# Optimization experiments

Measured on AMD Instinct MI355X. Metric: run time of the kernel, lower is better.

Reference implementation:

```python
import jax, jax.numpy as jnp
import numpy as np

K, D = 512, 64


def setup_inputs() -> dict:
    key = jax.random.key(0)
    k1, k2 = jax.random.split(key)
    z_e_x = jax.random.normal(k1, (32, 4096, D), dtype=jnp.float32)
    # nn.Embedding weight initialized uniform(-1/K, 1/K)
    codebook = jax.random.uniform(k2, (K, D), dtype=jnp.float32,
                                  minval=-1.0 / K, maxval=1.0 / K)
    return {"z_e_x": z_e_x, "codebook": codebook}


def reference(z_e_x, codebook):
    # vq(): pairwise squared L2 distances to codebook, then argmin.
    d = z_e_x.shape[-1]
    flat = z_e_x.reshape(-1, d)                                   # [N, D]
    # ||z||^2 - 2 z.e + ||e||^2  (addmm form from original vq)
    dists = (jnp.sum(flat * flat, axis=1, keepdims=True)
             - 2.0 * flat @ codebook.T
             + jnp.sum(codebook * codebook, axis=1))              # [N, K]
    indices = jnp.argmin(dists, axis=1)                            # [N]
    # latents: indices reshaped to input shape minus feature dim
    return indices.reshape(z_e_x.shape[:-1])
```

## Files before the change

kernel.cpp:

```cpp
#include <hip/hip_runtime.h>
#include <math.h>

#define K_CODES 512
#define D_DIM   64
#define BM      512
#define THREADS 512
#define LSTR    72
#define EPS_GAP 4e-5f

#define WS_CNT_OFF  2048
#define WS_EH_OFF   4096
#define WS_EL_OFF   77824
#define WS_LIST_OFF 151552

typedef __attribute__((ext_vector_type(8))) short short8v;
typedef __attribute__((ext_vector_type(4))) float f32x4;

__device__ __forceinline__ float np_sumsq64(const float* zarr) {
    float L[16];
#pragma unroll
    for (int j = 0; j < 16; ++j)
        L[j] = __fadd_rn(
            __fadd_rn(__fmul_rn(zarr[j],      zarr[j]),
                      __fmul_rn(zarr[j + 16], zarr[j + 16])),
            __fadd_rn(__fmul_rn(zarr[j + 32], zarr[j + 32]),
                      __fmul_rn(zarr[j + 48], zarr[j + 48])));
    float m[8];
#pragma unroll
    for (int j = 0; j < 8; ++j) m[j] = __fadd_rn(L[j], L[j + 8]);
    float n4[4];
#pragma unroll
    for (int j = 0; j < 4; ++j) n4[j] = __fadd_rn(m[j], m[j + 4]);
    return __fadd_rn(__fadd_rn(n4[0], n4[2]), __fadd_rn(n4[1], n4[3]));
}

__device__ __forceinline__ unsigned short f32_bf16_rne(float x) {
    unsigned int u = __float_as_uint(x);
    unsigned int r = (u + 0x7FFFu + ((u >> 16) & 1u)) >> 16;
    return (unsigned short)r;
}
__device__ __forceinline__ float bf16_f32(unsigned short h) {
    return __uint_as_float(((unsigned int)h) << 16);
}
__device__ __forceinline__ void split2(float x, unsigned short& h, unsigned short& l) {
    h = f32_bf16_rne(x);
    l = f32_bf16_rne(x - bf16_f32(h));
}

__global__ __launch_bounds__(256)
void vq_prep_kernel(const float* __restrict__ cb, float* __restrict__ ws,
                    int do_split) {
    int g = blockIdx.x * blockDim.x + threadIdx.x;
    if (g == 0) *reinterpret_cast<int*>((char*)ws + WS_CNT_OFF) = 0;
    int k = g >> 2, q = g & 3;
    if (k >= K_CODES) return;
    const float* row = cb + (size_t)k * D_DIM;
    if (q == 0) {
        float e[D_DIM];
        const float4* p = reinterpret_cast<const float4*>(row);
#pragma unroll
        for (int i = 0; i < 16; ++i) {
            float4 v = p[i];
            e[4*i+0]=v.x; e[4*i+1]=v.y; e[4*i+2]=v.z; e[4*i+3]=v.w;
        }
        ws[k] = np_sumsq64(e);
    }
    if (do_split) {
        unsigned short* eh = reinterpret_cast<unsigned short*>((char*)ws + WS_EH_OFF)
                             + (size_t)k * LSTR;
        unsigned short* el = reinterpret_cast<unsigned short*>((char*)ws + WS_EL_OFF)
                             + (size_t)k * LSTR;
#pragma unroll
        for (int i = 16 * q; i < 16 * q + 16; ++i) {
            unsigned short h, l;
            split2(row[i], h, l);
            eh[i] = h; el[i] = l;
        }
        if (q == 3)
#pragma unroll
            for (int i = D_DIM; i < LSTR; ++i) { eh[i] = 0; el[i] = 0; }
    }
}

__global__ __launch_bounds__(512)
void vq_pass1_mono(const float* __restrict__ z,
                   const unsigned short* __restrict__ eh_g,
                   const unsigned short* __restrict__ el_g,
                   const float* __restrict__ norms, int* __restrict__ out,
                   int* __restrict__ cnt, int* __restrict__ list, int cap, int n) {
    __shared__ __align__(16) unsigned short ehS[K_CODES * LSTR];
    __shared__ __align__(16) unsigned short elS[K_CODES * LSTR];
    __shared__ __align__(16) float nrmS[K_CODES];

    const int tid  = threadIdx.x;
    const int l    = tid & 63;
    const int w    = tid >> 6;
    const int j    = l >> 4;
    const int c16  = l & 15;
    const int base = blockIdx.x * BM;

    {
        const char* esrc = (const char*)eh_g;
        const char* lsrc = (const char*)el_g;
#pragma unroll
        for (int r = 0; r < 9; ++r) {
            size_t off = ((size_t)tid + (size_t)r * THREADS) * 16;
            __builtin_amdgcn_global_load_lds(
                (const __attribute__((address_space(1))) void*)(esrc + off),
                (__attribute__((address_space(3))) void*)((char*)ehS + off), 16, 0, 0);
            __builtin_amdgcn_global_load_lds(
                (const __attribute__((address_space(1))) void*)(lsrc + off),
                (__attribute__((address_space(3))) void*)((char*)elS + off), 16, 0, 0);
        }
        if (tid < K_CODES / 4)
            reinterpret_cast<float4*>(nrmS)[tid] =
                reinterpret_cast<const float4*>(norms)[tid];
    }

    short8v bzh[4][2], bzl[4][2];
#pragma unroll
    for (int p = 0; p < 4; ++p) {
        int row = base + (4 * w + p) * 16 + c16;
        if (row >= n) row = n - 1;
        const float* zp = z + (size_t)row * D_DIM + j * 8;
#pragma unroll
        for (int h = 0; h < 2; ++h) {
            float4 v0 = *reinterpret_cast<const float4*>(zp + h * 32);
            float4 v1 = *reinterpret_cast<const float4*>(zp + h * 32 + 4);
            unsigned short hh[8], ll[8];
            split2(v0.x, hh[0], ll[0]); split2(v0.y, hh[1], ll[1]);
            split2(v0.z, hh[2], ll[2]); split2(v0.w, hh[3], ll[3]);
            split2(v1.x, hh[4], ll[4]); split2(v1.y, hh[5], ll[5]);
            split2(v1.z, hh[6], ll[6]); split2(v1.w, hh[7], ll[7]);
            short8v th, tl;
#pragma unroll
            for (int i = 0; i < 8; ++i) { th[i] = (short)hh[i]; tl[i] = (short)ll[i]; }
            bzh[p][h] = th; bzl[p][h] = tl;
        }
    }

    __syncthreads();

    float m1[4] = {INFINITY, INFINITY, INFINITY, INFINITY};
    float m2[4] = {INFINITY, INFINITY, INFINITY, INFINITY};
    int   i1[4] = {0, 0, 0, 0};

#pragma unroll 4
    for (int ct = 0; ct < 32; ++ct) {
        int ar = (ct * 16 + c16) * LSTR + j * 8;
        short8v aeh0 = *reinterpret_cast<const short8v*>(&ehS[ar]);
        short8v aeh1 = *reinterpret_cast<const short8v*>(&ehS[ar + 32]);
        short8v ael0 = *reinterpret_cast<const short8v*>(&elS[ar]);
        short8v ael1 = *reinterpret_cast<const short8v*>(&elS[ar + 32]);
        float4 nr = *reinterpret_cast<const float4*>(&nrmS[ct * 16 + j * 4]);
        float nra[4] = {nr.x, nr.y, nr.z, nr.w};
        int kg0 = ct * 16 + j * 4;
#pragma unroll
        for (int p = 0; p < 4; ++p) {
            f32x4 acc = {0.f, 0.f, 0.f, 0.f};
            acc = __builtin_amdgcn_mfma_f32_16x16x32_bf16(aeh0, bzh[p][0], acc, 0, 0, 0);
            acc = __builtin_amdgcn_mfma_f32_16x16x32_bf16(aeh1, bzh[p][1], acc, 0, 0, 0);
            acc = __builtin_amdgcn_mfma_f32_16x16x32_bf16(aeh0, bzl[p][0], acc, 0, 0, 0);
            acc = __builtin_amdgcn_mfma_f32_16x16x32_bf16(aeh1, bzl[p][1], acc, 0, 0, 0);
            acc = __builtin_amdgcn_mfma_f32_16x16x32_bf16(ael0, bzh[p][0], acc, 0, 0, 0);
            acc = __builtin_amdgcn_mfma_f32_16x16x32_bf16(ael1, bzh[p][1], acc, 0, 0, 0);
#pragma unroll
            for (int r = 0; r < 4; ++r) {
                float s = fmaf(-2.0f, acc[r], nra[r]);
                int kg = kg0 + r;
                bool lt1 = s < m1[p];
                float nm2 = lt1 ? m1[p] : fminf(s, m2[p]);
                i1[p] = lt1 ? kg : i1[p];
                m1[p] = lt1 ? s : m1[p];
                m2[p] = nm2;
            }
        }
    }

#pragma unroll
    for (int p = 0; p < 4; ++p) {
        float a1 = m1[p], a2 = m2[p]; int ai = i1[p];
#pragma unroll
        for (int off = 16; off <= 32; off <<= 1) {
            float o1 = __shfl_xor(a1, off, 64);
            float o2 = __shfl_xor(a2, off, 64);
            int   oi = __shfl_xor(ai, off, 64);
            float hi = fmaxf(a1, o1);
            bool take = o1 < a1;
            ai = take ? oi : ai;
            a1 = take ? o1 : a1;
            a2 = fminf(hi, fminf(a2, o2));
        }
        int  ptg    = base + (4 * w + p) * 16 + c16;
        bool writer = (j == 0) && (ptg < n);
        bool flag   = writer && (a2 - a1 <= EPS_GAP);
        unsigned long long m = __ballot(flag);
        int abase = 0;
        if (m) {
            int leader = __ffsll(m) - 1;
            if (l == leader) abase = atomicAdd(cnt, __popcll(m));
            abase = __shfl(abase, leader, 64);
        }
        if (writer) {
            int val = ai;
            if (flag) {
                int rank = __popcll(m & ((1ull << l) - 1ull));
                int slot = abase + rank;
                if (slot < cap) list[slot] = ptg;
                else            val |= (int)0x80000000;
            }
            out[ptg] = val;
        }
    }
}

__global__ __launch_bounds__(256)
void vq_pass1_legacy(const float* __restrict__ z, const float* __restrict__ cb,
                     const float* __restrict__ norms, int* __restrict__ out,
                     int* __restrict__ cnt, int* __restrict__ list, int cap, int n) {
    __shared__ unsigned short zhS[128 * LSTR];
    __shared__ unsigned short zlS[128 * LSTR];
    __shared__ unsigned short ehS[128 * LSTR];
    __shared__ unsigned short elS[128 * LSTR];
    __shared__ float nrmL[128];

    const int tid  = threadIdx.x;
    const int l    = tid & 63;
    const int w    = tid >> 6;
    const int j    = l >> 4;
    const int c16  = l & 15;
    const int base = blockIdx.x * 128;

    const float4* z4 = reinterpret_cast<const float4*>(z);
#pragma unroll
    for (int rep = 0; rep < 8; ++rep) {
        int flat = rep * 256 + tid;
        int pt   = flat >> 4;
        int dblk = flat & 15;
        int gp = base + pt; if (gp >= n) gp = n - 1;
        float4 v = z4[(size_t)gp * 16 + dblk];
        ushort4 h, lo;
        split2(v.x, h.x, lo.x); split2(v.y, h.y, lo.y);
        split2(v.z, h.z, lo.z); split2(v.w, h.w, lo.w);
        *reinterpret_cast<ushort4*>(&zhS[pt * LSTR + dblk * 4]) = h;
        *reinterpret_cast<ushort4*>(&zlS[pt * LSTR + dblk * 4]) = lo;
    }
    __syncthreads();

    short8v bzh[2][2], bzl[2][2];
#pragma unroll
    for (int p = 0; p < 2; ++p) {
        int pr = ((2 * w + p) * 16 + c16) * LSTR;
#pragma unroll
        for (int h = 0; h < 2; ++h) {
            int off = pr + h * 32 + j * 8;
            bzh[p][h] = *reinterpret_cast<const short8v*>(&zhS[off]);
            bzl[p][h] = *reinterpret_cast<const short8v*>(&zlS[off]);
        }
    }

    float m1[2] = {INFINITY, INFINITY};
    float m2[2] = {INFINITY, INFINITY};
    int   i1[2] = {0, 0};

    for (int c = 0; c < 4; ++c) {
        __syncthreads();
        const float4* cb4 = reinterpret_cast<const float4*>(cb);
#pragma unroll
        for (int rep = 0; rep < 8; ++rep) {
            int flat = rep * 256 + tid;
            int code = flat >> 4;
            int dblk = flat & 15;
            float4 v = cb4[(size_t)(c * 128 + code) * 16 + dblk];
            ushort4 h, lo;
            split2(v.x, h.x, lo.x); split2(v.y, h.y, lo.y);
            split2(v.z, h.z, lo.z); split2(v.w, h.w, lo.w);
            *reinterpret_cast<ushort4*>(&ehS[code * LSTR + dblk * 4]) = h;
            *reinterpret_cast<ushort4*>(&elS[code * LSTR + dblk * 4]) = lo;
        }
        if (tid < 32)
            reinterpret_cast<float4*>(nrmL)[tid] =
                reinterpret_cast<const float4*>(norms)[c * 32 + tid];
        __syncthreads();

#pragma unroll
        for (int ct = 0; ct < 8; ++ct) {
            int ar = (ct * 16 + c16) * LSTR + j * 8;
            short8v aeh0 = *reinterpret_cast<const short8v*>(&ehS[ar]);
            short8v aeh1 = *reinterpret_cast<const short8v*>(&ehS[ar + 32]);
            short8v ael0 = *reinterpret_cast<const short8v*>(&elS[ar]);
            short8v ael1 = *reinterpret_cast<const short8v*>(&elS[ar + 32]);
            float4 nr = *reinterpret_cast<const float4*>(&nrmL[ct * 16 + j * 4]);
            float nra[4] = {nr.x, nr.y, nr.z, nr.w};
            int kg0 = c * 128 + ct * 16 + j * 4;
#pragma unroll
            for (int p = 0; p < 2; ++p) {
                f32x4 acc = {0.f, 0.f, 0.f, 0.f};
                acc = __builtin_amdgcn_mfma_f32_16x16x32_bf16(aeh0, bzh[p][0], acc, 0, 0, 0);
                acc = __builtin_amdgcn_mfma_f32_16x16x32_bf16(aeh1, bzh[p][1], acc, 0, 0, 0);
                acc = __builtin_amdgcn_mfma_f32_16x16x32_bf16(aeh0, bzl[p][0], acc, 0, 0, 0);
                acc = __builtin_amdgcn_mfma_f32_16x16x32_bf16(aeh1, bzl[p][1], acc, 0, 0, 0);
                acc = __builtin_amdgcn_mfma_f32_16x16x32_bf16(ael0, bzh[p][0], acc, 0, 0, 0);
                acc = __builtin_amdgcn_mfma_f32_16x16x32_bf16(ael1, bzh[p][1], acc, 0, 0, 0);
#pragma unroll
                for (int r = 0; r < 4; ++r) {
                    float s = fmaf(-2.0f, acc[r], nra[r]);
                    int kg = kg0 + r;
                    bool lt1 = s < m1[p];
                    float nm2 = lt1 ? m1[p] : fminf(s, m2[p]);
                    i1[p] = lt1 ? kg : i1[p];
                    m1[p] = lt1 ? s : m1[p];
                    m2[p] = nm2;
                }
            }
        }
    }

#pragma unroll
    for (int p = 0; p < 2; ++p) {
        float a1 = m1[p], a2 = m2[p]; int ai = i1[p];
#pragma unroll
        for (int off = 16; off <= 32; off <<= 1) {
            float o1 = __shfl_xor(a1, off, 64);
            float o2 = __shfl_xor(a2, off, 64);
            int   oi = __shfl_xor(ai, off, 64);
            float hi = fmaxf(a1, o1);
            bool take = o1 < a1;
            ai = take ? oi : ai;
            a1 = take ? o1 : a1;
            a2 = fminf(hi, fminf(a2, o2));
        }
        int  ptg    = base + (2 * w + p) * 16 + c16;
        bool writer = (j == 0) && (ptg < n);
        bool flag   = writer && (a2 - a1 <= EPS_GAP);
        unsigned long long m = __ballot(flag);
        int abase = 0;
        if (m) {
            int leader = __ffsll(m) - 1;
            if (l == leader) abase = atomicAdd(cnt, __popcll(m));
            abase = __shfl(abase, leader, 64);
        }
        if (writer) {
            int val = ai;
            if (flag) {
                int rank = __popcll(m & ((1ull << l) - 1ull));
                int slot = abase + rank;
                if (slot < cap) list[slot] = ptg;
                else            val |= (int)0x80000000;
            }
            out[ptg] = val;
        }
    }
}

__global__ __launch_bounds__(256)
void vq_cleanup_kernel(const float* __restrict__ z, const float* __restrict__ cb,
                       const float* __restrict__ norms,
                       const int* __restrict__ cnt, const int* __restrict__ list,
                       int cap, int* __restrict__ out, int n) {
    __shared__ float rbv[4];
    __shared__ int   rbi[4];
    const int tid  = threadIdx.x;
    const int lane = tid & 63;
    const int wv   = tid >> 6;

    int total = *cnt;
    int lim   = total < cap ? total : cap;

    for (int i = blockIdx.x; i < lim; i += gridDim.x) {
        int pt = list[i];
        float zr[D_DIM];
        const float4* zp = reinterpret_cast<const float4*>(z + (size_t)pt * D_DIM);
#pragma unroll
        for (int g = 0; g < 16; ++g) {
            float4 q = zp[g];
            zr[4*g+0]=q.x; zr[4*g+1]=q.y; zr[4*g+2]=q.z; zr[4*g+3]=q.w;
        }
        const float sz = np_sumsq64(zr);
        float best = INFINITY; int bi = 0x7FFFFFFF;
#pragma unroll 1
        for (int r = 0; r < 2; ++r) {
            int k = tid * 2 + r;
            const float4* e4 = reinterpret_cast<const float4*>(cb) + ((size_t)k << 4);
            float a = 0.f;
#pragma unroll
            for (int g = 0; g < 16; ++g) {
                float4 q = e4[g];
                a = fmaf(zr[4*g+0], q.x, a);
                a = fmaf(zr[4*g+1], q.y, a);
                a = fmaf(zr[4*g+2], q.z, a);
                a = fmaf(zr[4*g+3], q.w, a);
            }
            float s = __fadd_rn(__fsub_rn(sz, __fmul_rn(2.0f, a)), norms[k]);
            if (s < best || (s == best && k < bi)) { best = s; bi = k; }
        }
#pragma unroll
        for (int off = 1; off < 64; off <<= 1) {
            float os = __shfl_xor(best, off, 64);
            int   ok = __shfl_xor(bi, off, 64);
            if (os < best || (os == best && ok < bi)) { best = os; bi = ok; }
        }
        if (lane == 0) { rbv[wv] = best; rbi[wv] = bi; }
        __syncthreads();
        if (tid == 0) {
            float b = rbv[0]; int id = rbi[0];
#pragma unroll
            for (int q = 1; q < 4; ++q) {
                float v = rbv[q]; int vi = rbi[q];
                if (v < b || (v == b && vi < id)) { b = v; id = vi; }
            }
            out[pt] = id;
        }
        __syncthreads();
    }

    if (total > cap) {
        const int wid    = (blockIdx.x * blockDim.x + tid) >> 6;
        const int nwaves = (gridDim.x * blockDim.x) >> 6;
        for (int b = wid * 64; b < n; b += nwaves * 64) {
            int t = b + lane;
            int v = (t < n) ? out[t] : 0;
            unsigned long long m = __ballot(v < 0);
            while (m) {
                int bb = __ffsll(m) - 1;
                m &= m - 1ull;
                int pt = b + bb;
                float zr[D_DIM];
                const float4* zp = reinterpret_cast<const float4*>(z + (size_t)pt * D_DIM);
#pragma unroll
                for (int g = 0; g < 16; ++g) {
                    float4 q = zp[g];
                    zr[4*g+0]=q.x; zr[4*g+1]=q.y; zr[4*g+2]=q.z; zr[4*g+3]=q.w;
                }
                const float sz = np_sumsq64(zr);
                float best = INFINITY; int bi = 0x7FFFFFFF;
#pragma unroll 1
                for (int r = 0; r < 8; ++r) {
                    const float4* e4 = reinterpret_cast<const float4*>(cb) +
                                       ((size_t)(lane * 8 + r) << 4);
                    float a = 0.f;
#pragma unroll
                    for (int g = 0; g < 16; ++g) {
                        float4 q = e4[g];
                        a = fmaf(zr[4*g+0], q.x, a);
                        a = fmaf(zr[4*g+1], q.y, a);
                        a = fmaf(zr[4*g+2], q.z, a);
                        a = fmaf(zr[4*g+3], q.w, a);
                    }
                    float s = __fadd_rn(__fsub_rn(sz, __fmul_rn(2.0f, a)),
                                        norms[lane * 8 + r]);
                    if (s < best) { best = s; bi = lane * 8 + r; }
                }
#pragma unroll
                for (int off = 1; off < 64; off <<= 1) {
                    float os = __shfl_xor(best, off, 64);
                    int   ok = __shfl_xor(bi, off, 64);
                    if (os < best || (os == best && ok < bi)) { best = os; bi = ok; }
                }
                if (lane == 0) out[pt] = bi;
            }
        }
    }
}

extern "C" void kernel_launch(void* const* d_in, const int* in_sizes, int n_in,
                              void* d_out, int out_size, void* d_ws, size_t ws_size,
                              hipStream_t stream) {
    const float* z  = (const float*)d_in[0];
    const float* cb = (const float*)d_in[1];
    int n = in_sizes[0] / D_DIM;
    float* norms = (float*)d_ws;
    int*   cnt   = (int*)((char*)d_ws + WS_CNT_OFF);
    int* out = (int*)d_out;

    bool fast = ws_size >= (size_t)WS_LIST_OFF + 4096;
    vq_prep_kernel<<<(4 * K_CODES + 255) / 256, 256, 0, stream>>>(cb, norms, fast ? 1 : 0);

    if (fast) {
        const unsigned short* eh = (const unsigned short*)((char*)d_ws + WS_EH_OFF);
        const unsigned short* el = (const unsigned short*)((char*)d_ws + WS_EL_OFF);
        int* list = (int*)((char*)d_ws + WS_LIST_OFF);
        int  cap  = (int)((ws_size - WS_LIST_OFF) / 4);
        vq_pass1_mono<<<(n + BM - 1) / BM, THREADS, 0, stream>>>(
            z, eh, el, norms, out, cnt, list, cap, n);
        vq_cleanup_kernel<<<2048, 256, 0, stream>>>(z, cb, norms, cnt, list, cap, out, n);
    } else {
        int* list = (int*)d_ws + 513;
        int  cap  = (int)(ws_size / 4) - 513; if (cap < 0) cap = 0;
        vq_pass1_legacy<<<(n + 127) / 128, 256, 0, stream>>>(
            z, cb, norms, out, cnt, list, cap, n);
        vq_cleanup_kernel<<<2048, 256, 0, stream>>>(z, cb, norms, cnt, list, cap, out, n);
    }
}
```

Measured before the change: 61.00 us.

## Software-pipeline MFMA tiles against argmin epilogue with split accumulators

The code-tile loop is restructured into an even/odd ping-pong: the MFMAs for the next 16-code tile are issued while the running-argmin epilogue of the previous tile runs. The six dependent MFMAs per point group are split into two independent accumulator chains and interleaved across the four point groups, with s_setprio raised around the MFMA block. Each wave also starts at a rotated tile index so waves do not all hit the same LDS rows at once. The intent is to hide MFMA latency and VALU epilogue cost. In exchange it uses more VGPRs for the doubled accumulators, and tie ordering and fp summation order change slightly; the existing near-tie gap flag is meant to cover that.

```diff
diff --git a/kernel.cpp b/kernel.cpp
--- a/kernel.cpp
+++ b/kernel.cpp
@@ -82,6 +82,61 @@
     }
 }
 
+__device__ __forceinline__ void epi4(const f32x4& aA, const f32x4& aB,
+                                     const float4& nr, int kg0,
+                                     float& m1, float& m2, int& i1) {
+    float nra[4] = {nr.x, nr.y, nr.z, nr.w};
+#pragma unroll
+    for (int r = 0; r < 4; ++r) {
+        float dot = aA[r] + aB[r];
+        float s   = fmaf(-2.0f, dot, nra[r]);
+        bool lt1  = s < m1;
+        m2 = fminf(m2, fmaxf(m1, s));
+        i1 = lt1 ? (kg0 + r) : i1;
+        m1 = fminf(m1, s);
+    }
+}
+
+#define TILE_COMPUTE(CT, A0,A1,A2,A3, B0,B1,B2,B3, NR, KG)                       \
+  {                                                                              \
+    const int ct_ = (CT);                                                        \
+    int ar_ = (ct_ * 16 + c16) * LSTR + j * 8;                                   \
+    short8v aeh0_ = *reinterpret_cast<const short8v*>(&ehS[ar_]);                \
+    short8v aeh1_ = *reinterpret_cast<const short8v*>(&ehS[ar_ + 32]);           \
+    short8v ael0_ = *reinterpret_cast<const short8v*>(&elS[ar_]);                \
+    short8v ael1_ = *reinterpret_cast<const short8v*>(&elS[ar_ + 32]);           \
+    NR = *reinterpret_cast<const float4*>(&nrmS[ct_ * 16 + j * 4]);              \
+    KG = ct_ * 16 + j * 4;                                                       \
+    A0 = ZERO4; A1 = ZERO4; A2 = ZERO4; A3 = ZERO4;                              \
+    B0 = ZERO4; B1 = ZERO4; B2 = ZERO4; B3 = ZERO4;                              \
+    __builtin_amdgcn_s_setprio(1);                                               \
+    A0 = __builtin_amdgcn_mfma_f32_16x16x32_bf16(aeh0_, bzh[0][0], A0, 0,0,0);   \
+    A1 = __builtin_amdgcn_mfma_f32_16x16x32_bf16(aeh0_, bzh[1][0], A1, 0,0,0);   \
+    A2 = __builtin_amdgcn_mfma_f32_16x16x32_bf16(aeh0_, bzh[2][0], A2, 0,0,0);   \
+    A3 = __builtin_amdgcn_mfma_f32_16x16x32_bf16(aeh0_, bzh[3][0], A3, 0,0,0);   \
+    B0 = __builtin_amdgcn_mfma_f32_16x16x32_bf16(aeh1_, bzh[0][1], B0, 0,0,0);   \
+    B1 = __builtin_amdgcn_mfma_f32_16x16x32_bf16(aeh1_, bzh[1][1], B1, 0,0,0);   \
+    B2 = __builtin_amdgcn_mfma_f32_16x16x32_bf16(aeh1_, bzh[2][1], B2, 0,0,0);   \
+    B3 = __builtin_amdgcn_mfma_f32_16x16x32_bf16(aeh1_, bzh[3][1], B3, 0,0,0);   \
+    A0 = __builtin_amdgcn_mfma_f32_16x16x32_bf16(aeh0_, bzl[0][0], A0, 0,0,0);   \
+    A1 = __builtin_amdgcn_mfma_f32_16x16x32_bf16(aeh0_, bzl[1][0], A1, 0,0,0);   \
+    A2 = __builtin_amdgcn_mfma_f32_16x16x32_bf16(aeh0_, bzl[2][0], A2, 0,0,0);   \
+    A3 = __builtin_amdgcn_mfma_f32_16x16x32_bf16(aeh0_, bzl[3][0], A3, 0,0,0);   \
+    B0 = __builtin_amdgcn_mfma_f32_16x16x32_bf16(aeh1_, bzl[0][1], B0, 0,0,0);   \
+    B1 = __builtin_amdgcn_mfma_f32_16x16x32_bf16(aeh1_, bzl[1][1], B1, 0,0,0);   \
+    B2 = __builtin_amdgcn_mfma_f32_16x16x32_bf16(aeh1_, bzl[2][1], B2, 0,0,0);   \
+    B3 = __builtin_amdgcn_mfma_f32_16x16x32_bf16(aeh1_, bzl[3][1], B3, 0,0,0);   \
+    A0 = __builtin_amdgcn_mfma_f32_16x16x32_bf16(ael0_, bzh[0][0], A0, 0,0,0);   \
+    A1 = __builtin_amdgcn_mfma_f32_16x16x32_bf16(ael0_, bzh[1][0], A1, 0,0,0);   \
+    A2 = __builtin_amdgcn_mfma_f32_16x16x32_bf16(ael0_, bzh[2][0], A2, 0,0,0);   \
+    A3 = __builtin_amdgcn_mfma_f32_16x16x32_bf16(ael0_, bzh[3][0], A3, 0,0,0);   \
+    B0 = __builtin_amdgcn_mfma_f32_16x16x32_bf16(ael1_, bzh[0][1], B0, 0,0,0);   \
+    B1 = __builtin_amdgcn_mfma_f32_16x16x32_bf16(ael1_, bzh[1][1], B1, 0,0,0);   \
+    B2 = __builtin_amdgcn_mfma_f32_16x16x32_bf16(ael1_, bzh[2][1], B2, 0,0,0);   \
+    B3 = __builtin_amdgcn_mfma_f32_16x16x32_bf16(ael1_, bzh[3][1], B3, 0,0,0);   \
+    __builtin_amdgcn_s_setprio(0);                                               \
+  }
+
 __global__ __launch_bounds__(512)
 void vq_pass1_mono(const float* __restrict__ z,
                    const unsigned short* __restrict__ eh_g,
@@ -98,6 +153,7 @@
     const int j    = l >> 4;
     const int c16  = l & 15;
     const int base = blockIdx.x * BM;
+    const f32x4 ZERO4 = {0.f, 0.f, 0.f, 0.f};
 
     {
         const char* esrc = (const char*)eh_g;
@@ -145,37 +201,35 @@
     float m2[4] = {INFINITY, INFINITY, INFINITY, INFINITY};
     int   i1[4] = {0, 0, 0, 0};
 
-#pragma unroll 4
-    for (int ct = 0; ct < 32; ++ct) {
-        int ar = (ct * 16 + c16) * LSTR + j * 8;
-        short8v aeh0 = *reinterpret_cast<const short8v*>(&ehS[ar]);
-        short8v aeh1 = *reinterpret_cast<const short8v*>(&ehS[ar + 32]);
-        short8v ael0 = *reinterpret_cast<const short8v*>(&elS[ar]);
-        short8v ael1 = *reinterpret_cast<const short8v*>(&elS[ar + 32]);
-        float4 nr = *reinterpret_cast<const float4*>(&nrmS[ct * 16 + j * 4]);
-        float nra[4] = {nr.x, nr.y, nr.z, nr.w};
-        int kg0 = ct * 16 + j * 4;
-#pragma unroll
-        for (int p = 0; p < 4; ++p) {
-            f32x4 acc = {0.f, 0.f, 0.f, 0.f};
-            acc = __builtin_amdgcn_mfma_f32_16x16x32_bf16(aeh0, bzh[p][0], acc, 0, 0, 0);
-            acc = __builtin_amdgcn_mfma_f32_16x16x32_bf16(aeh1, bzh[p][1], acc, 0, 0, 0);
-            acc = __builtin_amdgcn_mfma_f32_16x16x32_bf16(aeh0, bzl[p][0], acc, 0, 0, 0);
-            acc = __builtin_amdgcn_mfma_f32_16x16x32_bf16(aeh1, bzl[p][1], acc, 0, 0, 0);
-            acc = __builtin_amdgcn_mfma_f32_16x16x32_bf16(ael0, bzh[p][0], acc, 0, 0, 0);
-            acc = __builtin_amdgcn_mfma_f32_16x16x32_bf16(ael1, bzh[p][1], acc, 0, 0, 0);
-#pragma unroll
-            for (int r = 0; r < 4; ++r) {
-                float s = fmaf(-2.0f, acc[r], nra[r]);
-                int kg = kg0 + r;
-                bool lt1 = s < m1[p];
-                float nm2 = lt1 ? m1[p] : fminf(s, m2[p]);
-                i1[p] = lt1 ? kg : i1[p];
-                m1[p] = lt1 ? s : m1[p];
-                m2[p] = nm2;
-            }
-        }
-    }
+#define CTMAP(X) (((X) + 4 * w) & 31)
+    f32x4 eA0,eA1,eA2,eA3,eB0,eB1,eB2,eB3;
+    f32x4 oA0,oA1,oA2,oA3,oB0,oB1,oB2,oB3;
+    float4 nrE, nrO; int kgE, kgO;
+
+    TILE_COMPUTE(CTMAP(0), eA0,eA1,eA2,eA3, eB0,eB1,eB2,eB3, nrE, kgE);
+#pragma unroll 1
+    for (int i = 0; i < 15; ++i) {
+        TILE_COMPUTE(CTMAP(2*i+1), oA0,oA1,oA2,oA3, oB0,oB1,oB2,oB3, nrO, kgO);
+        epi4(eA0, eB0, nrE, kgE, m1[0], m2[0], i1[0]);
+        epi4(eA1, eB1, nrE, kgE, m1[1], m2[1], i1[1]);
+        epi4(eA2, eB2, nrE, kgE, m1[2], m2[2], i1[2]);
+        epi4(eA3, eB3, nrE, kgE, m1[3], m2[3], i1[3]);
+        TILE_COMPUTE(CTMAP(2*i+2), eA0,eA1,eA2,eA3, eB0,eB1,eB2,eB3, nrE, kgE);
+        epi4(oA0, oB0, nrO, kgO, m1[0], m2[0], i1[0]);
+        epi4(oA1, oB1, nrO, kgO, m1[1], m2[1], i1[1]);
+        epi4(oA2, oB2, nrO, kgO, m1[2], m2[2], i1[2]);
+        epi4(oA3, oB3, nrO, kgO, m1[3], m2[3], i1[3]);
+    }
+    TILE_COMPUTE(CTMAP(31), oA0,oA1,oA2,oA3, oB0,oB1,oB2,oB3, nrO, kgO);
+    epi4(eA0, eB0, nrE, kgE, m1[0], m2[0], i1[0]);
+    epi4(eA1, eB1, nrE, kgE, m1[1], m2[1], i1[1]);
+    epi4(eA2, eB2, nrE, kgE, m1[2], m2[2], i1[2]);
+    epi4(eA3, eB3, nrE, kgE, m1[3], m2[3], i1[3]);
+    epi4(oA0, oB0, nrO, kgO, m1[0], m2[0], i1[0]);
+    epi4(oA1, oB1, nrO, kgO, m1[1], m2[1], i1[1]);
+    epi4(oA2, oB2, nrO, kgO, m1[2], m2[2], i1[2]);
+    epi4(oA3, oB3, nrO, kgO, m1[3], m2[3], i1[3]);
+#undef CTMAP
 
 #pragma unroll
     for (int p = 0; p < 4; ++p) {
```

Measured after the change: 64.10 us. 1.05x slower.
